# Kernel optimization log

Hardware: AMD Instinct MI355X
Metric: run time of the kernel (lower is better)

The kernel has to match this reference:

```python
import jax, jax.numpy as jnp
import numpy as np
from jax import lax

GRID = 32
CELLDAN = 4
D_NUM = GRID // CELLDAN          # 8 cells per axis
JUDGE = CELLDAN // 2             # half-window
B, P = 1024, D_NUM ** 3          # primNum = 512


def setup_inputs() -> dict:
    key = jax.random.key(0)
    ks = jax.random.split(key, 5)
    shape_rlt = jax.random.uniform(ks[0], (B, P, 3), dtype=jnp.float32)
    trans_rlt = jax.random.normal(ks[1], (B, P, 3), dtype=jnp.float32)
    quat_rlt = jax.random.normal(ks[2], (B, P, 4), dtype=jnp.float32)
    confi_rlt = jax.random.uniform(ks[3], (B, P, 1), dtype=jnp.float32)
    batchVolume = jax.random.randint(ks[4], (B, GRID, GRID, GRID), 0, 2, dtype=jnp.int32)
    return {"shape_rlt": shape_rlt, "trans_rlt": trans_rlt, "quat_rlt": quat_rlt,
            "confi_rlt": confi_rlt, "batchVolume": batchVolume}


def _iou_gt(batchVolume):
    # occupancy in {0,1}; original checks Volume[i][a][b][c] == 1 in a window
    # [c - judge, c + judge] (inclusive, clipped to grid) around each cell center.
    occ = (batchVolume == 1).astype(jnp.float32)
    win = 2 * JUDGE + 1
    # windowed "any" == max-pool with zero padding (clipping == pad with 0)
    pooled = lax.reduce_window(
        occ, 0.0, lax.max,
        window_dimensions=(1, win, win, win),
        window_strides=(1, 1, 1, 1),
        padding=[(0, 0)] + [(JUDGE, JUDGE)] * 3)
    centers = np.arange(D_NUM) * CELLDAN + CELLDAN // 2  # cell-center voxel coords
    sub = pooled[:, centers][:, :, centers][:, :, :, centers]  # [B, x, y, z]
    # j = z*d^2 + y*d + x  ->  flatten with x fastest
    iou = jnp.transpose(sub, (0, 3, 2, 1)).reshape(B, P)
    return iou


def reference(shape_rlt, trans_rlt, quat_rlt, confi_rlt, batchVolume):
    iou_gt = _iou_gt(batchVolume)                # [B, P] float, in {0., 1.}
    in_use = iou_gt.astype(jnp.int32)            # [B, P] int
    confi = jnp.squeeze(confi_rlt, axis=-1)      # [B, P]
    return confi, iou_gt, in_use
```

## Files before the change

### kernel.cpp

```cpp
#include <hip/hip_runtime.h>


constexpr int PN = 512;

__global__ __launch_bounds__(512) void confi_iou_kernel(
    const float* __restrict__ confi,
    const int*   __restrict__ vol,
    float*       __restrict__ out,
    int B)
{
    const int b = blockIdx.x;
    const int t = threadIdx.x;

    __shared__ unsigned short msh16[32][33];
    __shared__ unsigned short colOr16[8][33];
    __shared__ unsigned short fin16[8][8];

    const int* vb = vol + (size_t)b * 32768;

    const int q     = t & 255;
    const int i2row = q >> 3;
    const int half  = t >> 8;
    const int jrow  = (t >> 3) & 7;
    const bool writer = (t & 7) == 0;

    const int4* p = reinterpret_cast<const int4*>(vb) + half * 256 + q;

    #pragma unroll 4
    for (int it = 0; it < 16; ++it) {
        const int4 v = p[it * 512];
        const bool any4  = (v.x | v.y | v.z | v.w) != 0;
        const bool first = v.x != 0;
        const unsigned long long ma = __ballot(any4);
        const unsigned long long mb = __ballot(first);
        if (writer) {
            const unsigned a  = (unsigned)(ma >> (8 * jrow)) & 0xFFu;
            const unsigned bb = (unsigned)(mb >> (8 * jrow)) & 0xFFu;
            msh16[i2row][it * 2 + half] = (unsigned short)(a | (bb << 8));
        }
    }
    __syncthreads();

    if (t < 256) {
        const int c2 = t >> 5;
        const int i1 = t & 31;
        const int lo = 4 * c2;
        const int hi = (lo + 4 < 31) ? (lo + 4) : 31;
        unsigned acc = 0;
        #pragma unroll
        for (int i2 = lo; i2 <= hi; ++i2) acc |= msh16[i2][i1];
        colOr16[c2][i1] = (unsigned short)acc;
    }
    __syncthreads();

    if (t < 64) {
        const int c1 = t >> 3;
        const int c2 = t & 7;
        const int lo = 4 * c1;
        const int hi = (lo + 4 < 31) ? (lo + 4) : 31;
        unsigned acc = 0;
        #pragma unroll
        for (int i1 = lo; i1 <= hi; ++i1) acc |= colOr16[c2][i1];
        fin16[c1][c2] = (unsigned short)acc;
    }
    __syncthreads();

    {
        const int j  = t;
        const int c1 = j & 7;
        const int c2 = (j >> 3) & 7;
        const int c3 = j >> 6;
        const unsigned f  = fin16[c1][c2];
        const unsigned a  = f & 0xFFu;
        const unsigned bb = (f >> 8);
        const unsigned w = a | (bb >> 1);
        const float iou = ((w >> c3) & 1u) ? 1.0f : 0.0f;
        const int BP  = B * PN;
        const int idx = b * PN + j;
        out[idx]          = confi[idx];
        out[BP + idx]     = iou;
        out[2 * BP + idx] = iou;
    }
}

extern "C" void kernel_launch(void* const* d_in, const int* in_sizes, int n_in,
                              void* d_out, int out_size, void* d_ws, size_t ws_size,
                              hipStream_t stream) {
    const float* confi = (const float*)d_in[3];
    const int*   vol   = (const int*)d_in[4];
    float*       out   = (float*)d_out;
    const int B = in_sizes[4] / 32768;
    confi_iou_kernel<<<B, 512, 0, stream>>>(confi, vol, out, B);
}
```

Measured before the change: 27.03 us.

## Pre-reduce groups of four rows in registers to cut ballots and a reduction stage

Each thread now loads 16 int4 values and ORs them into per-group masks in registers, keeping separate masks for the group's first row so the boundary row of the next window can be added back in. Fewer ballot and shared-memory writes are needed, and one shared reduction stage plus one barrier are removed. All loads are issued up front (fully unrolled), which raises memory-level parallelism but also register pressure. The last stage now combines adjacent groups using the stored first-row masks.

```diff
diff --git a/kernel.cpp b/kernel.cpp
--- a/kernel.cpp
+++ b/kernel.cpp
@@ -12,56 +12,56 @@
     const int b = blockIdx.x;
     const int t = threadIdx.x;
 
-    __shared__ unsigned short msh16[32][33];
-    __shared__ unsigned short colOr16[8][33];
-    __shared__ unsigned short fin16[8][8];
+    __shared__ unsigned qmask[8][33];
+    __shared__ unsigned colQ[8][9];
 
     const int* vb = vol + (size_t)b * 32768;
+    const int q     = t & 255;
+    const int gbase = (t >> 8) * 4;
+    const int4* p = reinterpret_cast<const int4*>(vb) + gbase * 1024 + q;
 
-    const int q     = t & 255;
-    const int i2row = q >> 3;
-    const int half  = t >> 8;
-    const int jrow  = (t >> 3) & 7;
-    const bool writer = (t & 7) == 0;
+    unsigned qa[4], qf[4], sa[4], sf[4];
+    #pragma unroll
+    for (int g = 0; g < 4; ++g) {
+        qa[g] = 0; qf[g] = 0; sa[g] = 0; sf[g] = 0;
+        #pragma unroll
+        for (int s = 0; s < 4; ++s) {
+            const int4 v = p[(g * 4 + s) * 256];
+            const unsigned any = (unsigned)(v.x | v.y | v.z | v.w);
+            const unsigned fst = (unsigned)v.x;
+            qa[g] |= any; qf[g] |= fst;
+            if (s == 0) { sa[g] = any; sf[g] = fst; }
+        }
+    }
 
-    const int4* p = reinterpret_cast<const int4*>(vb) + half * 256 + q;
-
-    #pragma unroll 4
-    for (int it = 0; it < 16; ++it) {
-        const int4 v = p[it * 512];
-        const bool any4  = (v.x | v.y | v.z | v.w) != 0;
-        const bool first = v.x != 0;
-        const unsigned long long ma = __ballot(any4);
-        const unsigned long long mb = __ballot(first);
-        if (writer) {
-            const unsigned a  = (unsigned)(ma >> (8 * jrow)) & 0xFFu;
-            const unsigned bb = (unsigned)(mb >> (8 * jrow)) & 0xFFu;
-            msh16[i2row][it * 2 + half] = (unsigned short)(a | (bb << 8));
+    const int jrow   = (t >> 3) & 7;
+    const bool wr    = (t & 7) == 0;
+    const int i2row  = q >> 3;
+    #pragma unroll
+    for (int g = 0; g < 4; ++g) {
+        const unsigned long long ba = __ballot(qa[g] != 0);
+        const unsigned long long bf = __ballot(qf[g] != 0);
+        const unsigned long long bs = __ballot(sa[g] != 0);
+        const unsigned long long bt = __ballot(sf[g] != 0);
+        if (wr) {
+            const unsigned A = (unsigned)(ba >> (8 * jrow)) & 0xFFu;
+            const unsigned F = (unsigned)(bf >> (8 * jrow)) & 0xFFu;
+            const unsigned S = (unsigned)(bs >> (8 * jrow)) & 0xFFu;
+            const unsigned T = (unsigned)(bt >> (8 * jrow)) & 0xFFu;
+            qmask[gbase + g][i2row] = A | (F << 8) | (S << 16) | (T << 24);
         }
     }
     __syncthreads();
 
-    if (t < 256) {
-        const int c2 = t >> 5;
-        const int i1 = t & 31;
+    if (t < 64) {
+        const int g  = t >> 3;
+        const int c2 = t & 7;
         const int lo = 4 * c2;
         const int hi = (lo + 4 < 31) ? (lo + 4) : 31;
         unsigned acc = 0;
         #pragma unroll
-        for (int i2 = lo; i2 <= hi; ++i2) acc |= msh16[i2][i1];
-        colOr16[c2][i1] = (unsigned short)acc;
-    }
-    __syncthreads();
-
-    if (t < 64) {
-        const int c1 = t >> 3;
-        const int c2 = t & 7;
-        const int lo = 4 * c1;
-        const int hi = (lo + 4 < 31) ? (lo + 4) : 31;
-        unsigned acc = 0;
-        #pragma unroll
-        for (int i1 = lo; i1 <= hi; ++i1) acc |= colOr16[c2][i1];
-        fin16[c1][c2] = (unsigned short)acc;
+        for (int i2 = lo; i2 <= hi; ++i2) acc |= qmask[g][i2];
+        colQ[g][c2] = acc;
     }
     __syncthreads();
 
@@ -70,11 +70,12 @@
         const int c1 = j & 7;
         const int c2 = (j >> 3) & 7;
         const int c3 = j >> 6;
-        const unsigned f  = fin16[c1][c2];
-        const unsigned a  = f & 0xFFu;
-        const unsigned bb = (f >> 8);
-        const unsigned w = a | (bb >> 1);
-        const float iou = ((w >> c3) & 1u) ? 1.0f : 0.0f;
+        const unsigned u  = colQ[c1][c2];
+        const unsigned un = (c1 < 7) ? colQ[c1 + 1][c2] : 0u;
+        const unsigned RA = (u & 0xFFu)        | ((un >> 16) & 0xFFu);
+        const unsigned RF = ((u >> 8) & 0xFFu) | ((un >> 24) & 0xFFu);
+        const unsigned W  = RA | (RF >> 1);
+        const float iou = ((W >> c3) & 1u) ? 1.0f : 0.0f;
         const int BP  = B * PN;
         const int idx = b * PN + j;
         out[idx]          = confi[idx];
```

New measurement: 26.97 us. No clear change (-0.2%).
